# Kernel optimization log

Hardware: AMD Instinct MI355X
Metric: run time of the kernel (lower is better)

The kernel has to match this reference:

```python
import jax, jax.numpy as jnp
import numpy as np

N = 10000        # nodes
E = 160000       # edges
H = 256          # hidden_dim
K = 20           # mixture components
NL = 5           # num_layers
NODE_F = 64      # node_feature_dim
NNT = 10         # num_node_types
NET = 5          # num_edge_types + 1


def setup_inputs() -> dict:
    key = jax.random.key(0)
    ks = iter(jax.random.split(key, 64))

    def nrm(shape, fan_in):
        return jax.random.normal(next(ks), shape, jnp.float32) * (1.0 / np.sqrt(fan_in))

    inp = {}
    inp["x"] = jax.random.normal(next(ks), (N, NODE_F), jnp.float32)
    inp["edge_attr"] = jax.random.normal(next(ks), (E,), jnp.float32)
    # embeddings (weights stored as [in, out])
    inp["neW"] = nrm((NODE_F, H), NODE_F); inp["neb"] = jnp.zeros((H,), jnp.float32)
    inp["eeW"] = nrm((1, H), 1);           inp["eeb"] = jnp.zeros((H,), jnp.float32)
    # per-layer message MLPs f, g (stacked over NL layers)
    inp["fW1"] = nrm((NL, 3 * H, H), 3 * H); inp["fb1"] = jnp.zeros((NL, H), jnp.float32)
    inp["fW2"] = nrm((NL, H, H), H);         inp["fb2"] = jnp.zeros((NL, H), jnp.float32)
    inp["gW1"] = nrm((NL, 3 * H, H), 3 * H); inp["gb1"] = jnp.zeros((NL, H), jnp.float32)
    inp["gW2"] = nrm((NL, H, H), H);         inp["gb2"] = jnp.zeros((NL, H), jnp.float32)
    # per-layer GRU (PyTorch layout: weight_ih [3H, 2H], weight_hh [3H, H], gate order r,z,n)
    inp["gru_wih"] = nrm((NL, 3 * H, 2 * H), 2 * H)
    inp["gru_whh"] = nrm((NL, 3 * H, H), H)
    inp["gru_bih"] = jnp.zeros((NL, 3 * H), jnp.float32)
    inp["gru_bhh"] = jnp.zeros((NL, 3 * H), jnp.float32)
    # mlp_alpha: 3H -> H -> K
    inp["aW1"] = nrm((3 * H, H), 3 * H); inp["ab1"] = jnp.zeros((H,), jnp.float32)
    inp["aW2"] = nrm((H, K), H);         inp["ab2"] = jnp.zeros((K,), jnp.float32)
    # node_pred: 2H -> H -> NNT
    inp["npW1"] = nrm((2 * H, H), 2 * H); inp["npb1"] = jnp.zeros((H,), jnp.float32)
    inp["npW2"] = nrm((H, NNT), H);       inp["npb2"] = jnp.zeros((NNT,), jnp.float32)
    # edge_pred: H -> H -> NET*K
    inp["epW1"] = nrm((H, H), H);          inp["epb1"] = jnp.zeros((H,), jnp.float32)
    inp["epW2"] = nrm((H, NET * K), H);    inp["epb2"] = jnp.zeros((NET * K,), jnp.float32)
    inp["edge_index"] = jax.random.randint(next(ks), (2, E), 0, N)
    inp["v_t"] = N - 1
    return inp


def reference(x, edge_attr, neW, neb, eeW, eeb,
              fW1, fb1, fW2, fb2, gW1, gb1, gW2, gb2,
              gru_wih, gru_whh, gru_bih, gru_bhh,
              aW1, ab1, aW2, ab2, npW1, npb1, npW2, npb2,
              epW1, epb1, epW2, epb2, edge_index, v_t):
    src = edge_index[0]  # x_j
    dst = edge_index[1]  # x_i (aggregation target)

    h_v = x @ neW + neb                       # [N, H]
    h_e = edge_attr[:, None] @ eeW + eeb      # [E, H]

    for l in range(NL):
        cat = jnp.concatenate([h_v[dst], h_v[src], h_e], axis=-1)   # [E, 3H]
        m = jax.nn.relu(cat @ fW1[l] + fb1[l]) @ fW2[l] + fb2[l]    # [E, H]
        a = jax.nn.relu(cat @ gW1[l] + gb1[l]) @ gW2[l] + gb2[l]    # [E, H]
        agg = jax.ops.segment_sum(m * a, dst, num_segments=N)       # [N, H]
        # nn.GRU over the node dimension as a sequence (unbatched input [N, 2H])
        gi = jnp.concatenate([h_v, agg], axis=-1) @ gru_wih[l].T + gru_bih[l]  # [N, 3H]
        whh, bhh = gru_whh[l], gru_bhh[l]

        def step(h, g):
            gh = whh @ h + bhh
            ir, iz, i_n = jnp.split(g, 3)
            hr, hz, hn = jnp.split(gh, 3)
            r = jax.nn.sigmoid(ir + hr)
            z = jax.nn.sigmoid(iz + hz)
            n = jnp.tanh(i_n + r * hn)
            h2 = (1.0 - z) * n + z * h
            return h2, h2

        _, h_v = jax.lax.scan(step, jnp.zeros((H,), h_v.dtype), gi)  # [N, H]

    ge = jnp.broadcast_to(jnp.mean(h_v, axis=0), h_v.shape)          # [N, H]
    np_in = jnp.concatenate([ge, h_v], axis=-1)                      # [N, 2H]
    node_pred = jax.nn.relu(np_in @ npW1 + npb1) @ npW2 + npb2       # [N, NNT]

    h_v_t = jnp.broadcast_to(h_v[v_t], h_v.shape)                    # [N, H]
    al_in = jnp.concatenate([ge, h_v_t, h_v], axis=-1)               # [N, 3H]
    alphas = jax.nn.relu(al_in @ aW1 + ab1) @ aW2 + ab2              # [N, K]
    alphas = jax.nn.softmax(jnp.sum(alphas, axis=0, keepdims=True), axis=1)  # [1, K]

    p_v = jax.nn.softmax(node_pred, axis=-1)
    log_theta = (jax.nn.relu(h_v @ epW1 + epb1) @ epW2 + epb2).reshape(N, NET, K)
    p_e = jnp.sum(alphas * jax.nn.softmax(log_theta, axis=1), axis=-1)  # [N, NET]
    return p_v, p_e
```

## Files before the change

### kernel.cpp

```cpp
#include <hip/hip_runtime.h>
#include <hip/hip_bf16.h>

#define NN 10000
#define NE 160000

typedef _Float16 half8 __attribute__((ext_vector_type(8)));
typedef _Float16 half2v __attribute__((ext_vector_type(2)));
typedef float f32x4 __attribute__((ext_vector_type(4)));

__device__ __forceinline__ f32x4 mfma_f16(half8 a, half8 b, f32x4 c){
  return __builtin_amdgcn_mfma_f32_16x16x32_f16(a, b, c, 0, 0, 0);
}

#if defined(__has_builtin)
#if __has_builtin(__builtin_amdgcn_fdot2)
#define HAS_FDOT2 1
#endif
#endif

__device__ __forceinline__ float fdot2f(half2v a, half2v b, float c){
#ifdef HAS_FDOT2
  return __builtin_amdgcn_fdot2(a, b, c, false);
#else
  return c + (float)a[0]*(float)b[0] + (float)a[1]*(float)b[1];
#endif
}

__global__ void zero_f32_kernel(float* __restrict__ p, int n){
  int i = blockIdx.x*blockDim.x + threadIdx.x;
  int st = gridDim.x*blockDim.x;
  for (; i < n; i += st) p[i] = 0.f;
}

__global__ void cast_f16_kernel(const float* __restrict__ a, _Float16* __restrict__ o, int n){
  int i = blockIdx.x*blockDim.x + threadIdx.x;
  int st = gridDim.x*blockDim.x;
  for (; i < n; i += st) o[i] = (_Float16)a[i];
}

__global__ void prep_w1t_kernel(const float* __restrict__ f, const float* __restrict__ g,
                                _Float16* __restrict__ fT, _Float16* __restrict__ gT){
  int i = blockIdx.x*256 + threadIdx.x;
  if (i >= 5*256*768) return;
  int l = i / (256*768); int r = i % (256*768);
  int c = r / 768; int k = r % 768;
  size_t s = (size_t)l*768*256 + (size_t)k*256 + c;
  fT[i] = (_Float16)f[s]; gT[i] = (_Float16)g[s];
}
__global__ void prep_w2t_kernel(const float* __restrict__ f, const float* __restrict__ g,
                                _Float16* __restrict__ fT, _Float16* __restrict__ gT){
  int i = blockIdx.x*256 + threadIdx.x;
  if (i >= 5*256*256) return;
  int l = i / (256*256); int r = i % (256*256);
  int c = r / 256; int k = r % 256;
  size_t s = (size_t)l*256*256 + (size_t)k*256 + c;
  fT[i] = (_Float16)f[s]; gT[i] = (_Float16)g[s];
}

__global__ void hist_kernel(const int* __restrict__ dst, int* __restrict__ cnt){
  int e = blockIdx.x*256 + threadIdx.x;
  if (e < NE) atomicAdd(&cnt[dst[e]], 1);
}

__global__ __launch_bounds__(1024) void scan_off_kernel(const int* __restrict__ cnt, int* __restrict__ cur){
  __shared__ int sA[1024];
  const int t = threadIdx.x;
  int run = 0;
  for (int ch = 0; ch < 10; ++ch){
    int idx = ch*1024 + t;
    int v = (idx < NN) ? cnt[idx] : 0;
    sA[t] = v;
    __syncthreads();
    for (int o = 1; o < 1024; o <<= 1){
      int add = (t >= o) ? sA[t-o] : 0;
      __syncthreads();
      sA[t] += add;
      __syncthreads();
    }
    if (idx < NN) cur[idx] = run + sA[t] - v;
    run += sA[1023];
    __syncthreads();
  }
}

__global__ void scatter_kernel(const int* __restrict__ eidx, const float* __restrict__ ea,
                               int* __restrict__ cur, int* __restrict__ srcS,
                               int* __restrict__ dstS, float* __restrict__ eaS){
  int e = blockIdx.x*256 + threadIdx.x;
  if (e < NE){
    int d = eidx[NE + e];
    int p = atomicAdd(&cur[d], 1);
    srcS[p] = eidx[e];
    dstS[p] = d;
    eaS[p]  = ea[e];
  }
}

__global__ __launch_bounds__(256) void embed_kernel(const float* __restrict__ x,
    const float* __restrict__ neW, const float* __restrict__ neb,
    float* __restrict__ hv, _Float16* __restrict__ hvf){
  __shared__ float sx[16*64];
  int rb = blockIdx.x*16, t = threadIdx.x;
  for (int i = t; i < 16*64; i += 256) sx[i] = x[(size_t)rb*64 + i];
  __syncthreads();
  float acc[16];
  float bb = neb[t];
  #pragma unroll
  for (int r = 0; r < 16; r++) acc[r] = bb;
  for (int c = 0; c < 64; c++){
    float w = neW[c*256 + t];
    #pragma unroll
    for (int r = 0; r < 16; r++) acc[r] += sx[r*64 + c]*w;
  }
  for (int r = 0; r < 16; r++){
    hv [(size_t)(rb+r)*256 + t] = acc[r];
    hvf[(size_t)(rb+r)*256 + t] = (_Float16)acc[r];
  }
}

__global__ __launch_bounds__(256, 2) void edge_mlp_kernel(
    const _Float16* __restrict__ hvf, const float* __restrict__ eaS,
    const int* __restrict__ srcS, const int* __restrict__ dstS,
    const float* __restrict__ eeW, const float* __restrict__ eeb,
    const _Float16* __restrict__ fW1T, const float* __restrict__ fb1,
    const _Float16* __restrict__ fW2T, const float* __restrict__ fb2,
    const _Float16* __restrict__ gW1T, const float* __restrict__ gb1,
    const _Float16* __restrict__ gW2T, const float* __restrict__ gb2,
    float* __restrict__ agg)
{
  extern __shared__ char smem[];
  _Float16* sHid = (_Float16*)smem;
  float* sProd = (float*)smem;
  float* sEW  = (float*)(smem + 64*264*2);
  float* sEB  = sEW + 256;
  int*   sDst = (int*)(sEB + 256);

  const int tid = threadIdx.x;
  const int wave = tid >> 6, lane = tid & 63;
  const int l15 = lane & 15, l4 = lane >> 4;
  const int eb = blockIdx.x*64;
  if (tid < 256){ sEW[tid] = eeW[tid]; sEB[tid] = eeb[tid]; }
  if (tid < 64)  sDst[tid] = dstS[eb + tid];
  int dd[4], ss[4]; float ea[4];
  #pragma unroll
  for (int rt = 0; rt < 4; rt++){
    int e = eb + rt*16 + l15;
    dd[rt] = dstS[e]; ss[rt] = srcS[e]; ea[rt] = eaS[e];
  }
  __syncthreads();
  const int colw = wave*64;
  const f32x4 zf = {0.f, 0.f, 0.f, 0.f};

  f32x4 accM[4][4], accA[4][4];
  #pragma unroll
  for (int a_ = 0; a_ < 4; a_++)
    #pragma unroll
    for (int b_ = 0; b_ < 4; b_++){ accM[a_][b_] = zf; accA[a_][b_] = zf; }

  {
    f32x4 acc[4][4];
    #pragma unroll
    for (int a_ = 0; a_ < 4; a_++)
      #pragma unroll
      for (int b_ = 0; b_ < 4; b_++) acc[a_][b_] = zf;
    #pragma unroll 1
    for (int kc = 0; kc < 24; ++kc){
      const int kk = kc*32 + l4*8;
      half8 aF[4];
      if (kc < 8){
        #pragma unroll
        for (int rt = 0; rt < 4; rt++) aF[rt] = *(const half8*)(hvf + (size_t)dd[rt]*256 + kk);
      } else if (kc < 16){
        #pragma unroll
        for (int rt = 0; rt < 4; rt++) aF[rt] = *(const half8*)(hvf + (size_t)ss[rt]*256 + (kk - 256));
      } else {
        const int q = kk - 512;
        #pragma unroll
        for (int rt = 0; rt < 4; rt++){
          half8 v;
          #pragma unroll
          for (int j = 0; j < 8; j++) v[j] = (_Float16)(ea[rt]*sEW[q+j] + sEB[q+j]);
          aF[rt] = v;
        }
      }
      half8 bF[4];
      #pragma unroll
      for (int ct = 0; ct < 4; ct++)
        bF[ct] = *(const half8*)(fW1T + (size_t)(colw + ct*16 + l15)*768 + kk);
      #pragma unroll
      for (int rt = 0; rt < 4; rt++)
        #pragma unroll
        for (int ct = 0; ct < 4; ct++)
          acc[rt][ct] = mfma_f16(aF[rt], bF[ct], acc[rt][ct]);
    }
    #pragma unroll
    for (int ct = 0; ct < 4; ct++){
      const int col = colw + ct*16 + l15;
      const float bb = fb1[col];
      #pragma unroll
      for (int rt = 0; rt < 4; rt++)
        #pragma unroll
        for (int ri = 0; ri < 4; ri++){
          int row = rt*16 + l4*4 + ri;
          sHid[row*264 + col] = (_Float16)fmaxf(acc[rt][ct][ri] + bb, 0.f);
        }
    }
    __syncthreads();
    #pragma unroll 1
    for (int kc = 0; kc < 8; ++kc){
      const int kk = kc*32 + l4*8;
      half8 aF[4], bF[4];
      #pragma unroll
      for (int rt = 0; rt < 4; rt++) aF[rt] = *(const half8*)(sHid + (rt*16 + l15)*264 + kk);
      #pragma unroll
      for (int ct = 0; ct < 4; ct++) bF[ct] = *(const half8*)(fW2T + (size_t)(colw + ct*16 + l15)*256 + kk);
      #pragma unroll
      for (int rt = 0; rt < 4; rt++)
        #pragma unroll
        for (int ct = 0; ct < 4; ct++)
          accM[rt][ct] = mfma_f16(aF[rt], bF[ct], accM[rt][ct]);
    }
    __syncthreads();
  }

  {
    f32x4 acc[4][4];
    #pragma unroll
    for (int a_ = 0; a_ < 4; a_++)
      #pragma unroll
      for (int b_ = 0; b_ < 4; b_++) acc[a_][b_] = zf;
    #pragma unroll 1
    for (int kc = 0; kc < 24; ++kc){
      const int kk = kc*32 + l4*8;
      half8 aF[4];
      if (kc < 8){
        #pragma unroll
        for (int rt = 0; rt < 4; rt++) aF[rt] = *(const half8*)(hvf + (size_t)dd[rt]*256 + kk);
      } else if (kc < 16){
        #pragma unroll
        for (int rt = 0; rt < 4; rt++) aF[rt] = *(const half8*)(hvf + (size_t)ss[rt]*256 + (kk - 256));
      } else {
        const int q = kk - 512;
        #pragma unroll
        for (int rt = 0; rt < 4; rt++){
          half8 v;
          #pragma unroll
          for (int j = 0; j < 8; j++) v[j] = (_Float16)(ea[rt]*sEW[q+j] + sEB[q+j]);
          aF[rt] = v;
        }
      }
      half8 bF[4];
      #pragma unroll
      for (int ct = 0; ct < 4; ct++)
        bF[ct] = *(const half8*)(gW1T + (size_t)(colw + ct*16 + l15)*768 + kk);
      #pragma unroll
      for (int rt = 0; rt < 4; rt++)
        #pragma unroll
        for (int ct = 0; ct < 4; ct++)
          acc[rt][ct] = mfma_f16(aF[rt], bF[ct], acc[rt][ct]);
    }
    #pragma unroll
    for (int ct = 0; ct < 4; ct++){
      const int col = colw + ct*16 + l15;
      const float bb = gb1[col];
      #pragma unroll
      for (int rt = 0; rt < 4; rt++)
        #pragma unroll
        for (int ri = 0; ri < 4; ri++){
          int row = rt*16 + l4*4 + ri;
          sHid[row*264 + col] = (_Float16)fmaxf(acc[rt][ct][ri] + bb, 0.f);
        }
    }
    __syncthreads();
    #pragma unroll 1
    for (int kc = 0; kc < 8; ++kc){
      const int kk = kc*32 + l4*8;
      half8 aF[4], bF[4];
      #pragma unroll
      for (int rt = 0; rt < 4; rt++) aF[rt] = *(const half8*)(sHid + (rt*16 + l15)*264 + kk);
      #pragma unroll
      for (int ct = 0; ct < 4; ct++) bF[ct] = *(const half8*)(gW2T + (size_t)(colw + ct*16 + l15)*256 + kk);
      #pragma unroll
      for (int rt = 0; rt < 4; rt++)
        #pragma unroll
        for (int ct = 0; ct < 4; ct++)
          accA[rt][ct] = mfma_f16(aF[rt], bF[ct], accA[rt][ct]);
    }
    __syncthreads();
  }

  int cd = sDst[0]; float ac = 0.f;
  #pragma unroll 1
  for (int hf = 0; hf < 2; ++hf){
    #pragma unroll
    for (int ct = 0; ct < 4; ct++){
      const int col = colw + ct*16 + l15;
      const float bm = fb2[col], ba = gb2[col];
      #pragma unroll
      for (int rt2 = 0; rt2 < 2; rt2++){
        const int rt = hf*2 + rt2;
        #pragma unroll
        for (int ri = 0; ri < 4; ri++){
          int row = rt2*16 + l4*4 + ri;
          sProd[row*264 + col] = (accM[rt][ct][ri] + bm)*(accA[rt][ct][ri] + ba);
        }
      }
    }
    __syncthreads();
    for (int r = 0; r < 32; ++r){
      float v = sProd[r*264 + tid];
      int dr = sDst[hf*32 + r];
      if (dr != cd){ atomicAdd(&agg[(size_t)cd*256 + tid], ac); ac = 0.f; cd = dr; }
      ac += v;
    }
    __syncthreads();
  }
  atomicAdd(&agg[(size_t)cd*256 + tid], ac);
}

#define RB_GI 157
__global__ __launch_bounds__(256, 3) void gi_mfma_kernel(
    const _Float16* __restrict__ hvf, const _Float16* __restrict__ aggf,
    const _Float16* __restrict__ wihL, const float* __restrict__ bihL,
    float* __restrict__ gi)
{
  const int tid = threadIdx.x;
  const int wave = tid >> 6, lane = tid & 63, l15 = lane & 15, l4 = lane >> 4;
  const int rblk = blockIdx.x % RB_GI;
  const int cg   = blockIdx.x / RB_GI;
  const int rb = rblk*64;
  const int colw = cg*256 + wave*64;
  int rowc[4];
  #pragma unroll
  for (int rt = 0; rt < 4; rt++){ int r = rb + rt*16 + l15; rowc[rt] = (r < NN) ? r : NN-1; }
  const f32x4 zf = {0.f, 0.f, 0.f, 0.f};
  f32x4 acc[4][4];
  #pragma unroll
  for (int a_ = 0; a_ < 4; a_++)
    #pragma unroll
    for (int b_ = 0; b_ < 4; b_++) acc[a_][b_] = zf;
  #pragma unroll 1
  for (int kc = 0; kc < 16; ++kc){
    const int kk = kc*32 + l4*8;
    half8 aF[4], bF[4];
    if (kc < 8){
      #pragma unroll
      for (int rt = 0; rt < 4; rt++) aF[rt] = *(const half8*)(hvf + (size_t)rowc[rt]*256 + kk);
    } else {
      #pragma unroll
      for (int rt = 0; rt < 4; rt++) aF[rt] = *(const half8*)(aggf + (size_t)rowc[rt]*256 + (kk - 256));
    }
    #pragma unroll
    for (int ct = 0; ct < 4; ct++)
      bF[ct] = *(const half8*)(wihL + (size_t)(colw + ct*16 + l15)*512 + kk);
    #pragma unroll
    for (int rt = 0; rt < 4; rt++)
      #pragma unroll
      for (int ct = 0; ct < 4; ct++)
        acc[rt][ct] = mfma_f16(aF[rt], bF[ct], acc[rt][ct]);
  }
  #pragma unroll
  for (int ct = 0; ct < 4; ct++){
    const int col = colw + ct*16 + l15;
    const float bb = bihL[col];
    #pragma unroll
    for (int rt = 0; rt < 4; rt++)
      #pragma unroll
      for (int ri = 0; ri < 4; ri++){
        int row = rb + rt*16 + l4*4 + ri;
        if (row < NN) gi[(size_t)row*768 + col] = acc[rt][ct][ri] + bb;
      }
  }
}

#define FOR16(M) M(0) M(1) M(2) M(3) M(4) M(5) M(6) M(7) M(8) M(9) M(10) M(11) M(12) M(13) M(14) M(15)

#define DECL_W(i) half8 wr##i, wz##i, wn##i;

#define LD8(dst, q, i) { float4 _a = (q)[2*(i)], _b = (q)[2*(i)+1]; \
  dst[0]=(_Float16)_a.x; dst[1]=(_Float16)_a.y; dst[2]=(_Float16)_a.z; dst[3]=(_Float16)_a.w; \
  dst[4]=(_Float16)_b.x; dst[5]=(_Float16)_b.y; dst[6]=(_Float16)_b.z; dst[7]=(_Float16)_b.w; }

#define LOAD_W(i) LD8(wr##i, q0, i) LD8(wz##i, q1, i) LD8(wn##i, q2, i)

#define OPQ(i) asm volatile("" : "+v"(wr##i), "+v"(wz##i), "+v"(wn##i));

#define SV(w, a, b) __builtin_shufflevector(w, w, a, b)

#define DOT_STEP(i) { half8 hh = ph[i]; \
  half2v h0 = SV(hh, 0, 1), h1 = SV(hh, 2, 3), h2 = SV(hh, 4, 5), h3 = SV(hh, 6, 7); \
  ar0 = fdot2f(SV(wr##i, 0, 1), h0, ar0); ar1 = fdot2f(SV(wr##i, 2, 3), h1, ar1); \
  ar0 = fdot2f(SV(wr##i, 4, 5), h2, ar0); ar1 = fdot2f(SV(wr##i, 6, 7), h3, ar1); \
  az0 = fdot2f(SV(wz##i, 0, 1), h0, az0); az1 = fdot2f(SV(wz##i, 2, 3), h1, az1); \
  az0 = fdot2f(SV(wz##i, 4, 5), h2, az0); az1 = fdot2f(SV(wz##i, 6, 7), h3, az1); \
  an0 = fdot2f(SV(wn##i, 0, 1), h0, an0); an1 = fdot2f(SV(wn##i, 2, 3), h1, an1); \
  an0 = fdot2f(SV(wn##i, 4, 5), h2, an0); an1 = fdot2f(SV(wn##i, 6, 7), h3, an1); }

__global__ __launch_bounds__(512, 1) void gru_scan11(
    const float* __restrict__ whhL, const float* __restrict__ bhhL,
    const float* __restrict__ gi, float* __restrict__ hv, _Float16* __restrict__ hvf)
{
  const int t = threadIdx.x;
  const int row = t & 255;
  const int hf  = t >> 8;
  const int c0  = hf*128;
  FOR16(DECL_W)
  {
    const float4* q0 = (const float4*)(whhL + (size_t)row*256 + c0);
    const float4* q1 = (const float4*)(whhL + (size_t)(256 + row)*256 + c0);
    const float4* q2 = (const float4*)(whhL + (size_t)(512 + row)*256 + c0);
    FOR16(LOAD_W)
  }
  FOR16(OPQ)
  const float br = bhhL[row], bz = bhhL[256 + row], bn = bhhL[512 + row];
  __shared__ __align__(16) _Float16 sH16[256];
  __shared__ float sP[6][256];
  float h = 0.f;
  if (t < 256) sH16[t] = (_Float16)0.f;
  float gr = 0.f, gz = 0.f, gn = 0.f;
  if (t < 256){ gr = gi[t]; gz = gi[256 + t]; gn = gi[512 + t]; }
  __syncthreads();
  #pragma unroll 1
  for (int step = 0; step < NN; ++step){
    float pr = 0.f, pz = 0.f, pn = 0.f;
    if (t < 256){
      const float* g = gi + (size_t)((step + 1 < NN) ? step + 1 : step)*768;
      pr = g[t]; pz = g[256 + t]; pn = g[512 + t];
    }
    const half8* ph = (const half8*)(sH16 + c0);
    float ar0 = 0.f, ar1 = 0.f, az0 = 0.f, az1 = 0.f, an0 = 0.f, an1 = 0.f;
    FOR16(DOT_STEP)
    sP[0 + hf][row] = ar0 + ar1;
    sP[2 + hf][row] = az0 + az1;
    sP[4 + hf][row] = an0 + an1;
    __syncthreads();
    if (t < 256){
      float hr = sP[0][t] + sP[1][t] + br;
      float hz = sP[2][t] + sP[3][t] + bz;
      float hn = sP[4][t] + sP[5][t] + bn;
      float r = 1.f/(1.f + __expf(-(gr + hr)));
      float z = 1.f/(1.f + __expf(-(gz + hz)));
      float xx = gn + r*hn;
      xx = fminf(fmaxf(xx, -15.f), 15.f);
      float e2 = __expf(2.f*xx);
      float n = (e2 - 1.f)/(e2 + 1.f);
      h = n + z*(h - n);
      hv [(size_t)step*256 + t] = h;
      hvf[(size_t)step*256 + t] = (_Float16)h;
      sH16[t] = (_Float16)h;
      gr = pr; gz = pz; gn = pn;
    }
    __syncthreads();
  }
}

__global__ __launch_bounds__(256) void ge_sum_kernel(const float* __restrict__ hv, float* __restrict__ ge){
  int rb = blockIdx.x*40, t = threadIdx.x;
  float s = 0.f;
  for (int i = 0; i < 40; i++) s += hv[(size_t)(rb + i)*256 + t];
  atomicAdd(&ge[t], s);
}

__global__ void finalize_kernel(const float* __restrict__ ge, const float* __restrict__ hv,
                                const int* __restrict__ vt, float* __restrict__ gem, float* __restrict__ hvt){
  int t = threadIdx.x;
  gem[t] = ge[t]*(1.0f/NN);
  hvt[t] = hv[(size_t)vt[0]*256 + t];
}

__global__ __launch_bounds__(256) void base_np_kernel(const float* __restrict__ gem,
    const float* __restrict__ npW1, const float* __restrict__ npb1, float* __restrict__ bnp){
  __shared__ float sg[256];
  int t = threadIdx.x; sg[t] = gem[t]; __syncthreads();
  float a = npb1[t];
  for (int c = 0; c < 256; c++) a += sg[c]*npW1[c*256 + t];
  bnp[t] = a;
}

__global__ __launch_bounds__(256) void base_al_kernel(const float* __restrict__ gem,
    const float* __restrict__ hvt, const float* __restrict__ aW1,
    const float* __restrict__ ab1, float* __restrict__ bal){
  __shared__ float sg[256], sv[256];
  int t = threadIdx.x; sg[t] = gem[t]; sv[t] = hvt[t]; __syncthreads();
  float a = ab1[t];
  for (int c = 0; c < 256; c++) a += sg[c]*aW1[c*256 + t];
  for (int c = 0; c < 256; c++) a += sv[c]*aW1[(256 + c)*256 + t];
  bal[t] = a;
}

__global__ __launch_bounds__(256) void node_pred_kernel(const float* __restrict__ hv,
    const float* __restrict__ bnp, const float* __restrict__ npW1,
    const float* __restrict__ npW2, const float* __restrict__ npb2,
    float* __restrict__ outPV){
  __shared__ float sHv[16*256];
  __shared__ float sHid[16*257];
  __shared__ float sLg[16*10];
  int rb = blockIdx.x*16, t = threadIdx.x;
  for (int i = t; i < 4096; i += 256) sHv[i] = hv[(size_t)rb*256 + i];
  __syncthreads();
  float acc[16]; float b = bnp[t];
  #pragma unroll
  for (int r = 0; r < 16; r++) acc[r] = b;
  for (int c = 0; c < 256; c++){
    float w = npW1[(256 + c)*256 + t];
    #pragma unroll
    for (int r = 0; r < 16; r++) acc[r] += sHv[r*256 + c]*w;
  }
  for (int r = 0; r < 16; r++) sHid[r*257 + t] = fmaxf(acc[r], 0.f);
  __syncthreads();
  {
    int r = t >> 4, u = t & 15;
    if (u < 10){
      float a = npb2[u];
      for (int c = 0; c < 256; c++) a += sHid[r*257 + c]*npW2[c*10 + u];
      sLg[r*10 + u] = a;
    }
  }
  __syncthreads();
  if (t < 16){
    float mx = -1e30f;
    for (int u = 0; u < 10; u++) mx = fmaxf(mx, sLg[t*10 + u]);
    float s = 0.f, e[10];
    for (int u = 0; u < 10; u++){ e[u] = __expf(sLg[t*10 + u] - mx); s += e[u]; }
    float inv = 1.f/s;
    for (int u = 0; u < 10; u++) outPV[(size_t)(rb + t)*10 + u] = e[u]*inv;
  }
}

__global__ __launch_bounds__(256) void alphas_kernel(const float* __restrict__ hv,
    const float* __restrict__ bal, const float* __restrict__ aW1,
    const float* __restrict__ aW2, const float* __restrict__ ab2,
    float* __restrict__ alsum){
  __shared__ float sHv[16*256];
  __shared__ float sHid[16*257];
  __shared__ float sAv[16*20];
  int rb = blockIdx.x*16, t = threadIdx.x;
  for (int i = t; i < 4096; i += 256) sHv[i] = hv[(size_t)rb*256 + i];
  __syncthreads();
  float acc[16]; float b = bal[t];
  #pragma unroll
  for (int r = 0; r < 16; r++) acc[r] = b;
  for (int c = 0; c < 256; c++){
    float w = aW1[(512 + c)*256 + t];
    #pragma unroll
    for (int r = 0; r < 16; r++) acc[r] += sHv[r*256 + c]*w;
  }
  for (int r = 0; r < 16; r++) sHid[r*257 + t] = fmaxf(acc[r], 0.f);
  __syncthreads();
  {
    int r = t >> 4, k = t & 15;
    float a = ab2[k];
    for (int c = 0; c < 256; c++) a += sHid[r*257 + c]*aW2[c*20 + k];
    sAv[r*20 + k] = a;
    if (k < 4){
      int k2 = 16 + k;
      float a2 = ab2[k2];
      for (int c = 0; c < 256; c++) a2 += sHid[r*257 + c]*aW2[c*20 + k2];
      sAv[r*20 + k2] = a2;
    }
  }
  __syncthreads();
  if (t < 20){
    float s = 0.f;
    for (int rr = 0; rr < 16; rr++) s += sAv[rr*20 + t];
    atomicAdd(&alsum[t], s);
  }
}

__global__ void alpha_softmax_kernel(const float* __restrict__ alsum, float* __restrict__ alph){
  if (threadIdx.x == 0){
    float mx = -1e30f;
    for (int k = 0; k < 20; k++) mx = fmaxf(mx, alsum[k]);
    float s = 0.f, e[20];
    for (int k = 0; k < 20; k++){ e[k] = __expf(alsum[k] - mx); s += e[k]; }
    for (int k = 0; k < 20; k++) alph[k] = e[k]/s;
  }
}

__global__ __launch_bounds__(256) void edge_pred_kernel(const float* __restrict__ hv,
    const float* __restrict__ epW1, const float* __restrict__ epb1,
    const float* __restrict__ epW2, const float* __restrict__ epb2,
    const float* __restrict__ alph, float* __restrict__ outPE){
  __shared__ float sHv[16*256];
  __shared__ float sHid[16*257];
  __shared__ float sLT[16*100];
  __shared__ float sPE[16*5];
  __shared__ float sAl[20];
  int rb = blockIdx.x*16, t = threadIdx.x;
  for (int i = t; i < 4096; i += 256) sHv[i] = hv[(size_t)rb*256 + i];
  if (t < 20) sAl[t] = alph[t];
  if (t < 80) sPE[t] = 0.f;
  __syncthreads();
  float acc[16]; float b = epb1[t];
  #pragma unroll
  for (int r = 0; r < 16; r++) acc[r] = b;
  for (int c = 0; c < 256; c++){
    float w = epW1[c*256 + t];
    #pragma unroll
    for (int r = 0; r < 16; r++) acc[r] += sHv[r*256 + c]*w;
  }
  for (int r = 0; r < 16; r++) sHid[r*257 + t] = fmaxf(acc[r], 0.f);
  __syncthreads();
  for (int p = 0; p < 7; p++){
    int idx = p*256 + t;
    if (idx < 1600){
      int r = idx/100, j = idx%100;
      float a = epb2[j];
      for (int c = 0; c < 256; c++) a += sHid[r*257 + c]*epW2[c*100 + j];
      sLT[r*100 + j] = a;
    }
  }
  __syncthreads();
  {
    int r = t >> 4, k = t & 15;
    for (int pass = 0; pass < 2; ++pass){
      int kk = pass ? (16 + k) : k;
      if (pass && k >= 4) break;
      float lt[5];
      #pragma unroll
      for (int net = 0; net < 5; net++) lt[net] = sLT[r*100 + net*20 + kk];
      float mx = lt[0];
      #pragma unroll
      for (int net = 1; net < 5; net++) mx = fmaxf(mx, lt[net]);
      float e[5], s = 0.f;
      #pragma unroll
      for (int net = 0; net < 5; net++){ e[net] = __expf(lt[net] - mx); s += e[net]; }
      float wgt = sAl[kk]/s;
      #pragma unroll
      for (int net = 0; net < 5; net++) atomicAdd(&sPE[r*5 + net], e[net]*wgt);
    }
  }
  __syncthreads();
  if (t < 80){
    int r = t/5, net = t%5;
    outPE[(size_t)(rb + r)*5 + net] = sPE[t];
  }
}

extern "C" void kernel_launch(void* const* d_in, const int* in_sizes, int n_in,
                              void* d_out, int out_size, void* d_ws, size_t ws_size,
                              hipStream_t stream){
  const float* x    = (const float*)d_in[0];
  const float* edge_attr = (const float*)d_in[1];
  const float* neW  = (const float*)d_in[2];
  const float* neb  = (const float*)d_in[3];
  const float* eeW  = (const float*)d_in[4];
  const float* eeb  = (const float*)d_in[5];
  const float* fW1  = (const float*)d_in[6];
  const float* fb1  = (const float*)d_in[7];
  const float* fW2  = (const float*)d_in[8];
  const float* fb2  = (const float*)d_in[9];
  const float* gW1  = (const float*)d_in[10];
  const float* gb1  = (const float*)d_in[11];
  const float* gW2  = (const float*)d_in[12];
  const float* gb2  = (const float*)d_in[13];
  const float* wih  = (const float*)d_in[14];
  const float* whh  = (const float*)d_in[15];
  const float* bih  = (const float*)d_in[16];
  const float* bhh  = (const float*)d_in[17];
  const float* aW1  = (const float*)d_in[18];
  const float* ab1  = (const float*)d_in[19];
  const float* aW2  = (const float*)d_in[20];
  const float* ab2  = (const float*)d_in[21];
  const float* npW1 = (const float*)d_in[22];
  const float* npb1 = (const float*)d_in[23];
  const float* npW2 = (const float*)d_in[24];
  const float* npb2 = (const float*)d_in[25];
  const float* epW1 = (const float*)d_in[26];
  const float* epb1 = (const float*)d_in[27];
  const float* epW2 = (const float*)d_in[28];
  const float* epb2 = (const float*)d_in[29];
  const int*   eidx = (const int*)d_in[30];
  const int*   vt   = (const int*)d_in[31];

  char* ws = (char*)d_ws;
  size_t off_ = 0;
  auto alloc = [&](size_t b){ size_t r = off_; off_ += (b + 511) & ~(size_t)511; return r; };
  float*    hv    = (float*)   (ws + alloc((size_t)NN*256*4));
  _Float16* hvf   = (_Float16*)(ws + alloc((size_t)NN*256*2));
  float*    agg   = (float*)   (ws + alloc((size_t)NN*256*4));
  _Float16* aggf  = (_Float16*)(ws + alloc((size_t)NN*256*2));
  float*    gi    = (float*)   (ws + alloc((size_t)NN*768*4));
  _Float16* fW1T  = (_Float16*)(ws + alloc((size_t)5*256*768*2));
  _Float16* gW1T  = (_Float16*)(ws + alloc((size_t)5*256*768*2));
  _Float16* fW2T  = (_Float16*)(ws + alloc((size_t)5*256*256*2));
  _Float16* gW2T  = (_Float16*)(ws + alloc((size_t)5*256*256*2));
  _Float16* wihf  = (_Float16*)(ws + alloc((size_t)5*768*512*2));
  int*      cnt   = (int*)     (ws + alloc((size_t)NN*4));
  int*      cur   = (int*)     (ws + alloc((size_t)NN*4));
  int*      srcS  = (int*)     (ws + alloc((size_t)NE*4));
  int*      dstS  = (int*)     (ws + alloc((size_t)NE*4));
  float*    eaS   = (float*)   (ws + alloc((size_t)NE*4));
  float*    ge    = (float*)   (ws + alloc(256*4));
  float*    gem   = (float*)   (ws + alloc(256*4));
  float*    hvt   = (float*)   (ws + alloc(256*4));
  float*    bnp   = (float*)   (ws + alloc(256*4));
  float*    bal   = (float*)   (ws + alloc(256*4));
  float*    alsum = (float*)   (ws + alloc(128));
  float*    alph  = (float*)   (ws + alloc(128));

  float* outPV = (float*)d_out;
  float* outPE = outPV + (size_t)NN*10;

  prep_w1t_kernel<<<3840, 256, 0, stream>>>(fW1, gW1, fW1T, gW1T);
  prep_w2t_kernel<<<1280, 256, 0, stream>>>(fW2, gW2, fW2T, gW2T);
  cast_f16_kernel<<<2048, 256, 0, stream>>>(wih, wihf, 5*768*512);

  zero_f32_kernel<<<40, 256, 0, stream>>>((float*)cnt, NN);
  hist_kernel<<<625, 256, 0, stream>>>(eidx + NE, cnt);
  scan_off_kernel<<<1, 1024, 0, stream>>>(cnt, cur);
  scatter_kernel<<<625, 256, 0, stream>>>(eidx, edge_attr, cur, srcS, dstS, eaS);

  embed_kernel<<<625, 256, 0, stream>>>(x, neW, neb, hv, hvf);

  const size_t edge_lds = (size_t)64*264*2 + 2048 + 256;
  for (int l = 0; l < 5; ++l){
    zero_f32_kernel<<<2048, 256, 0, stream>>>(agg, NN*256);
    edge_mlp_kernel<<<2500, 256, edge_lds, stream>>>(hvf, eaS, srcS, dstS, eeW, eeb,
        fW1T + (size_t)l*256*768, fb1 + l*256, fW2T + (size_t)l*256*256, fb2 + l*256,
        gW1T + (size_t)l*256*768, gb1 + l*256, gW2T + (size_t)l*256*256, gb2 + l*256, agg);
    cast_f16_kernel<<<2048, 256, 0, stream>>>(agg, aggf, NN*256);
    gi_mfma_kernel<<<471, 256, 0, stream>>>(hvf, aggf, wihf + (size_t)l*768*512, bih + l*768, gi);
    gru_scan11<<<1, 512, 0, stream>>>(whh + (size_t)l*768*256, bhh + l*768, gi, hv, hvf);
  }

  zero_f32_kernel<<<1, 256, 0, stream>>>(ge, 256);
  zero_f32_kernel<<<1, 64, 0, stream>>>(alsum, 32);
  ge_sum_kernel<<<250, 256, 0, stream>>>(hv, ge);
  finalize_kernel<<<1, 256, 0, stream>>>(ge, hv, vt, gem, hvt);
  base_np_kernel<<<1, 256, 0, stream>>>(gem, npW1, npb1, bnp);
  base_al_kernel<<<1, 256, 0, stream>>>(gem, hvt, aW1, ab1, bal);
  node_pred_kernel<<<625, 256, 0, stream>>>(hv, bnp, npW1, npW2, npb2, outPV);
  alphas_kernel<<<625, 256, 0, stream>>>(hv, bal, aW1, aW2, ab2, alsum);
  alpha_softmax_kernel<<<1, 64, 0, stream>>>(alsum, alph);
  edge_pred_kernel<<<625, 256, 0, stream>>>(hv, epW1, epb1, epW2, epb2, alph, outPE);
}
```

Measured before the change: 57.80 ms.

## Restructure GRU scan to 768 threads with LDS-resident n-gate weights

Replaces the 512-thread GRU recurrence kernel, which held all recurrent weights in registers split across two half-rows, with a 768-thread kernel where each thread computes one full output row. The r and z gate rows stream from a prepacked fp16 global buffer (double-buffered loads, expected to hit L2), while the n gate rows are cached in XOR-swizzled LDS. This removes the cross-half partial-sum reduction and the heavy register pressure, at the cost of re-reading weights from cache/LDS on every one of the 10000 serial steps. A fallback to the old kernel runs if the launch fails.

```diff
diff --git a/kernel.cpp b/kernel.cpp
--- a/kernel.cpp
+++ b/kernel.cpp
@@ -55,6 +55,17 @@
   int c = r / 256; int k = r % 256;
   size_t s = (size_t)l*256*256 + (size_t)k*256 + c;
   fT[i] = (_Float16)f[s]; gT[i] = (_Float16)g[s];
+}
+
+__global__ void prep_whhPk_kernel(const float* __restrict__ whh, _Float16* __restrict__ pk){
+  int idx = blockIdx.x*256 + threadIdx.x;
+  if (idx >= 5*32*768) return;
+  int l = idx / (32*768); int r = idx % (32*768);
+  int i = r / 768; int t = r % 768;
+  const float* s = whh + (size_t)l*768*256 + (size_t)t*256 + i*8;
+  _Float16* d = pk + (size_t)idx*8;
+  #pragma unroll
+  for (int e = 0; e < 8; e++) d[e] = (_Float16)s[e];
 }
 
 __global__ void hist_kernel(const int* __restrict__ dst, int* __restrict__ cnt){
@@ -374,19 +385,13 @@
 }
 
 #define FOR16(M) M(0) M(1) M(2) M(3) M(4) M(5) M(6) M(7) M(8) M(9) M(10) M(11) M(12) M(13) M(14) M(15)
-
 #define DECL_W(i) half8 wr##i, wz##i, wn##i;
-
 #define LD8(dst, q, i) { float4 _a = (q)[2*(i)], _b = (q)[2*(i)+1]; \
   dst[0]=(_Float16)_a.x; dst[1]=(_Float16)_a.y; dst[2]=(_Float16)_a.z; dst[3]=(_Float16)_a.w; \
   dst[4]=(_Float16)_b.x; dst[5]=(_Float16)_b.y; dst[6]=(_Float16)_b.z; dst[7]=(_Float16)_b.w; }
-
 #define LOAD_W(i) LD8(wr##i, q0, i) LD8(wz##i, q1, i) LD8(wn##i, q2, i)
-
 #define OPQ(i) asm volatile("" : "+v"(wr##i), "+v"(wz##i), "+v"(wn##i));
-
 #define SV(w, a, b) __builtin_shufflevector(w, w, a, b)
-
 #define DOT_STEP(i) { half8 hh = ph[i]; \
   half2v h0 = SV(hh, 0, 1), h1 = SV(hh, 2, 3), h2 = SV(hh, 4, 5), h3 = SV(hh, 6, 7); \
   ar0 = fdot2f(SV(wr##i, 0, 1), h0, ar0); ar1 = fdot2f(SV(wr##i, 2, 3), h1, ar1); \
@@ -438,6 +443,96 @@
       float hr = sP[0][t] + sP[1][t] + br;
       float hz = sP[2][t] + sP[3][t] + bz;
       float hn = sP[4][t] + sP[5][t] + bn;
+      float r = 1.f/(1.f + __expf(-(gr + hr)));
+      float z = 1.f/(1.f + __expf(-(gz + hz)));
+      float xx = gn + r*hn;
+      xx = fminf(fmaxf(xx, -15.f), 15.f);
+      float e2 = __expf(2.f*xx);
+      float n = (e2 - 1.f)/(e2 + 1.f);
+      h = n + z*(h - n);
+      hv [(size_t)step*256 + t] = h;
+      hvf[(size_t)step*256 + t] = (_Float16)h;
+      sH16[t] = (_Float16)h;
+      gr = pr; gz = pz; gn = pn;
+    }
+    __syncthreads();
+  }
+}
+
+#define SVv(w, a, b) __builtin_shufflevector(w, w, a, b)
+#define DOT8(w, h, acc) { \
+  acc = fdot2f(SVv(w,0,1), SVv(h,0,1), acc); acc = fdot2f(SVv(w,2,3), SVv(h,2,3), acc); \
+  acc = fdot2f(SVv(w,4,5), SVv(h,4,5), acc); acc = fdot2f(SVv(w,6,7), SVv(h,6,7), acc); }
+#define LDPK(i) (*(const half8*)(pk + ((size_t)(i)*768 + t)*8))
+#define PHASE(p, C0, C1, C2, C3, N0, N1, N2, N3) { \
+  if ((p) < 7){ N0 = LDPK(4*(p)+4); N1 = LDPK(4*(p)+5); N2 = LDPK(4*(p)+6); N3 = LDPK(4*(p)+7); } \
+  half8 h0 = ph[4*(p)+0], h1 = ph[4*(p)+1], h2 = ph[4*(p)+2], h3 = ph[4*(p)+3]; \
+  DOT8(C0, h0, a0) DOT8(C1, h1, a1) DOT8(C2, h2, a2) DOT8(C3, h3, a3) }
+
+__global__ __launch_bounds__(768, 1) void gru_scan13(
+    const _Float16* __restrict__ pk,
+    const float* __restrict__ whhL,
+    const float* __restrict__ bhhL,
+    const float* __restrict__ gi, float* __restrict__ hv, _Float16* __restrict__ hvf)
+{
+  extern __shared__ char sm[];
+  half8* wnL = (half8*)sm;
+  float* sGH = (float*)(sm + 131072);
+  _Float16* sH16 = (_Float16*)(sm + 131072 + 3072);
+  const int t = threadIdx.x;
+  for (int idx = t; idx < 256*32; idx += 768){
+    int row = idx >> 5, j = idx & 31;
+    const float* s = whhL + (size_t)(512 + row)*256 + j*8;
+    half8 v;
+    #pragma unroll
+    for (int e = 0; e < 8; e++) v[e] = (_Float16)s[e];
+    wnL[(row << 5) | (j ^ (row & 7))] = v;
+  }
+  const float bh = bhhL[t];
+  float h = 0.f;
+  if (t < 256) sH16[t] = (_Float16)0.f;
+  float gr = 0.f, gz = 0.f, gn = 0.f;
+  if (t < 256){ gr = gi[t]; gz = gi[256 + t]; gn = gi[512 + t]; }
+  __syncthreads();
+  const bool isn = (t >= 512);
+  const int nrow = t - 512;
+  #pragma unroll 1
+  for (int step = 0; step < NN; ++step){
+    float pr = 0.f, pz = 0.f, pn = 0.f;
+    if (t < 256){
+      const float* g = gi + (size_t)((step + 1 < NN) ? step + 1 : step)*768;
+      pr = g[t]; pz = g[256 + t]; pn = g[512 + t];
+    }
+    const half8* ph = (const half8*)sH16;
+    float a0 = 0.f, a1 = 0.f, a2 = 0.f, a3 = 0.f;
+    if (!isn){
+      half8 Wa0 = LDPK(0), Wa1 = LDPK(1), Wa2 = LDPK(2), Wa3 = LDPK(3);
+      half8 Wb0, Wb1, Wb2, Wb3;
+      PHASE(0, Wa0, Wa1, Wa2, Wa3, Wb0, Wb1, Wb2, Wb3)
+      PHASE(1, Wb0, Wb1, Wb2, Wb3, Wa0, Wa1, Wa2, Wa3)
+      PHASE(2, Wa0, Wa1, Wa2, Wa3, Wb0, Wb1, Wb2, Wb3)
+      PHASE(3, Wb0, Wb1, Wb2, Wb3, Wa0, Wa1, Wa2, Wa3)
+      PHASE(4, Wa0, Wa1, Wa2, Wa3, Wb0, Wb1, Wb2, Wb3)
+      PHASE(5, Wb0, Wb1, Wb2, Wb3, Wa0, Wa1, Wa2, Wa3)
+      PHASE(6, Wa0, Wa1, Wa2, Wa3, Wb0, Wb1, Wb2, Wb3)
+      PHASE(7, Wb0, Wb1, Wb2, Wb3, Wa0, Wa1, Wa2, Wa3)
+    } else {
+      const half8* wr = wnL + (nrow << 5);
+      const int sw = nrow & 7;
+      #pragma unroll
+      for (int j = 0; j < 32; j += 4){
+        half8 w0 = wr[(j+0) ^ sw];
+        half8 w1 = wr[(j+1) ^ sw];
+        half8 w2 = wr[(j+2) ^ sw];
+        half8 w3 = wr[(j+3) ^ sw];
+        half8 h0 = ph[j+0], h1 = ph[j+1], h2 = ph[j+2], h3 = ph[j+3];
+        DOT8(w0, h0, a0) DOT8(w1, h1, a1) DOT8(w2, h2, a2) DOT8(w3, h3, a3)
+      }
+    }
+    sGH[t] = (a0 + a1) + (a2 + a3) + bh;
+    __syncthreads();
+    if (t < 256){
+      float hr = sGH[t], hz = sGH[256 + t], hn = sGH[512 + t];
       float r = 1.f/(1.f + __expf(-(gr + hr)));
       float z = 1.f/(1.f + __expf(-(gz + hz)));
       float xx = gn + r*hn;
@@ -686,6 +781,7 @@
   _Float16* fW2T  = (_Float16*)(ws + alloc((size_t)5*256*256*2));
   _Float16* gW2T  = (_Float16*)(ws + alloc((size_t)5*256*256*2));
   _Float16* wihf  = (_Float16*)(ws + alloc((size_t)5*768*512*2));
+  _Float16* whhPk = (_Float16*)(ws + alloc((size_t)5*32*768*8*2));
   int*      cnt   = (int*)     (ws + alloc((size_t)NN*4));
   int*      cur   = (int*)     (ws + alloc((size_t)NN*4));
   int*      srcS  = (int*)     (ws + alloc((size_t)NE*4));
@@ -702,9 +798,14 @@
   float* outPV = (float*)d_out;
   float* outPE = outPV + (size_t)NN*10;
 
+  (void)hipFuncSetAttribute((const void*)gru_scan13,
+                            hipFuncAttributeMaxDynamicSharedMemorySize, 135168);
+  (void)hipGetLastError();
+
   prep_w1t_kernel<<<3840, 256, 0, stream>>>(fW1, gW1, fW1T, gW1T);
   prep_w2t_kernel<<<1280, 256, 0, stream>>>(fW2, gW2, fW2T, gW2T);
   cast_f16_kernel<<<2048, 256, 0, stream>>>(wih, wihf, 5*768*512);
+  prep_whhPk_kernel<<<480, 256, 0, stream>>>(whh, whhPk);
 
   zero_f32_kernel<<<40, 256, 0, stream>>>((float*)cnt, NN);
   hist_kernel<<<625, 256, 0, stream>>>(eidx + NE, cnt);
@@ -714,6 +815,7 @@
   embed_kernel<<<625, 256, 0, stream>>>(x, neW, neb, hv, hvf);
 
   const size_t edge_lds = (size_t)64*264*2 + 2048 + 256;
+  const size_t gru_lds  = 131072 + 3072 + 512;
   for (int l = 0; l < 5; ++l){
     zero_f32_kernel<<<2048, 256, 0, stream>>>(agg, NN*256);
     edge_mlp_kernel<<<2500, 256, edge_lds, stream>>>(hvf, eaS, srcS, dstS, eeW, eeb,
@@ -721,7 +823,11 @@
         gW1T + (size_t)l*256*768, gb1 + l*256, gW2T + (size_t)l*256*256, gb2 + l*256, agg);
     cast_f16_kernel<<<2048, 256, 0, stream>>>(agg, aggf, NN*256);
     gi_mfma_kernel<<<471, 256, 0, stream>>>(hvf, aggf, wihf + (size_t)l*768*512, bih + l*768, gi);
-    gru_scan11<<<1, 512, 0, stream>>>(whh + (size_t)l*768*256, bhh + l*768, gi, hv, hvf);
+    gru_scan13<<<1, 768, gru_lds, stream>>>(whhPk + (size_t)l*32*768*8,
+        whh + (size_t)l*768*256, bhh + l*768, gi, hv, hvf);
+    if (hipGetLastError() != hipSuccess){
+      gru_scan11<<<1, 512, 0, stream>>>(whh + (size_t)l*768*256, bhh + l*768, gi, hv, hvf);
+    }
   }
 
   zero_f32_kernel<<<1, 256, 0, stream>>>(ge, 256);
```

Result: slower. 117.5 ms (+103.3%).
